# Performance work log

Measured on AMD Instinct MI355X. Metric: run time of the kernel, lower is better.

Reference implementation:

```python
import jax, jax.numpy as jnp
import numpy as np

NUM_EXPERTS = 64
TOP_K = 8
HIDDEN = 2048
MLP = 768
TOKENS = 1024


def setup_inputs() -> dict:
    key = jax.random.key(0)
    ks = jax.random.split(key, 5)
    hidden_states = jax.random.normal(ks[0], (TOKENS, HIDDEN), dtype=jnp.float32)
    # lecun-normal-ish scaling (std = 1/sqrt(fan_in))
    router_w = jax.random.normal(ks[1], (HIDDEN, NUM_EXPERTS), dtype=jnp.float32) / np.sqrt(HIDDEN)
    gate_proj = jax.random.normal(ks[2], (NUM_EXPERTS, HIDDEN, MLP), dtype=jnp.float32) / np.sqrt(HIDDEN)
    up_proj = jax.random.normal(ks[3], (NUM_EXPERTS, HIDDEN, MLP), dtype=jnp.float32) / np.sqrt(HIDDEN)
    down_proj = jax.random.normal(ks[4], (NUM_EXPERTS, MLP, HIDDEN), dtype=jnp.float32) / np.sqrt(MLP)
    return {
        "hidden_states": hidden_states,
        "router_w": router_w,
        "gate_proj": gate_proj,
        "up_proj": up_proj,
        "down_proj": down_proj,
    }


def reference(hidden_states, router_w, gate_proj, up_proj, down_proj):
    # Router: [T, E]
    router_logits = hidden_states @ router_w
    # Top-k routing, softmax renormalized over the selected k (norm_topk_prob=True)
    routing_weights, selected_experts = jax.lax.top_k(router_logits, k=TOP_K)
    routing_weights = jax.nn.softmax(routing_weights, axis=-1)  # [T, k]

    sel_flat = selected_experts.ravel()  # [T*k] int32
    # Duplicate each token for each of its k experts: [T*k, H]
    x_exp = jnp.repeat(hidden_states, TOP_K, axis=0)

    # prepare_routing: sort token copies by expert id, count per-expert group sizes
    sort_idx = jnp.argsort(sel_flat)          # stable sort of expert ids
    x_sorted = x_exp[sort_idx]                # [T*k, H] grouped by expert
    group_sizes = jnp.zeros((NUM_EXPERTS,), dtype=jnp.int32).at[sel_flat].add(1)
    unsort_idx = jnp.argsort(sort_idx)

    # Grouped GEMMs (megablox-style) via ragged_dot
    gate_out = jax.lax.ragged_dot(x_sorted, gate_proj, group_sizes)   # [T*k, M]
    up_out = jax.lax.ragged_dot(x_sorted, up_proj, group_sizes)       # [T*k, M]
    down_out = jax.lax.ragged_dot(jax.nn.silu(gate_out) * up_out, down_proj, group_sizes)  # [T*k, H]

    # Unsort back to (token, k) order and combine with routing weights
    unsorted = down_out[unsort_idx].reshape(-1, TOP_K, HIDDEN)
    return jnp.sum(unsorted * routing_weights[..., None], axis=1)  # [T, H]
```

## Files before the change

kernel.cpp:

```cpp
#include <hip/hip_runtime.h>
#include <hip/hip_bf16.h>

#define T_TOKENS 1024
#define HID      2048
#define NEXP     64
#define TOPK     8
#define MLP      768
#define NPAIR    (T_TOKENS * TOPK)

typedef __bf16 bf16x8 __attribute__((ext_vector_type(8)));
typedef float  f32x4  __attribute__((ext_vector_type(4)));
typedef unsigned int u32x2 __attribute__((ext_vector_type(2)));
typedef unsigned int u32x4 __attribute__((ext_vector_type(4)));

#define LDK 40

static __device__ __forceinline__ unsigned short f2bf(float f) {
    __hip_bfloat16 h = __float2bfloat16(f);
    unsigned short u;
    __builtin_memcpy(&u, &h, sizeof(u));
    return u;
}
static __device__ __forceinline__ unsigned int pk2bf(float a, float b) {
    return (unsigned int)f2bf(a) | ((unsigned int)f2bf(b) << 16);
}

__global__ __launch_bounds__(256) void router_topk_kernel(
    const float* __restrict__ hs, const float* __restrict__ rw,
    int* __restrict__ sel, float* __restrict__ wts, unsigned short* __restrict__ xb)
{
    const int lane = threadIdx.x & 63;
    const int tg   = threadIdx.x >> 6;
    const int t    = blockIdx.x * 4 + tg;

    {
        const float* xr = hs + (size_t)t * HID;
        unsigned short* xw = xb + (size_t)t * HID;
        #pragma unroll
        for (int c = 0; c < 4; ++c) {
            int i = (lane + c * 64) * 8;
            f32x4 a = *(const f32x4*)(xr + i);
            f32x4 b = *(const f32x4*)(xr + i + 4);
            u32x4 v;
            v[0] = pk2bf(a[0], a[1]); v[1] = pk2bf(a[2], a[3]);
            v[2] = pk2bf(b[0], b[1]); v[3] = pk2bf(b[2], b[3]);
            *(u32x4*)(xw + i) = v;
        }
    }

    const float4* x4 = (const float4*)(hs + (size_t)t * HID);
    float acc = 0.f;
    for (int h4 = 0; h4 < HID / 4; ++h4) {
        float4 xv = x4[h4];
        int hb = h4 * 4 * NEXP + lane;
        acc += xv.x * rw[hb] + xv.y * rw[hb + NEXP]
             + xv.z * rw[hb + 2 * NEXP] + xv.w * rw[hb + 3 * NEXP];
    }

    float v = acc;
    float tv[TOPK]; int ti[TOPK];
    for (int i = 0; i < TOPK; ++i) {
        float m = v; int mi = lane;
        for (int off = 32; off > 0; off >>= 1) {
            float om  = __shfl_xor(m, off, 64);
            int   omi = __shfl_xor(mi, off, 64);
            if (om > m || (om == m && omi < mi)) { m = om; mi = omi; }
        }
        tv[i] = m; ti[i] = mi;
        if (lane == mi) v = -__builtin_inff();
    }
    if (lane == 0) {
        float mx = tv[0], s = 0.f, e[TOPK];
        for (int i = 0; i < TOPK; ++i) { e[i] = __expf(tv[i] - mx); s += e[i]; }
        float inv = 1.f / s;
        for (int i = 0; i < TOPK; ++i) {
            wts[t * TOPK + i] = e[i] * inv;
            sel[t * TOPK + i] = ti[i];
        }
    }
}

__global__ __launch_bounds__(1024) void route_kernel(
    const int* __restrict__ sel, int* __restrict__ offsets, int* __restrict__ rows)
{
    __shared__ int cnt[NEXP];
    __shared__ int cur[NEXP];
    const int t = threadIdx.x;
    if (t < NEXP) cnt[t] = 0;
    __syncthreads();
    int e[8];
    const int p0 = t * 8;
    #pragma unroll
    for (int j = 0; j < 8; ++j) {
        e[j] = sel[p0 + j];
        atomicAdd(&cnt[e[j]], 1);
    }
    __syncthreads();
    if (t == 0) {
        int s = 0;
        for (int i = 0; i < NEXP; ++i) { cur[i] = s; offsets[i] = s; s += cnt[i]; }
        offsets[NEXP] = s;
    }
    __syncthreads();
    #pragma unroll
    for (int j = 0; j < 8; ++j) {
        int pos = atomicAdd(&cur[e[j]], 1);
        rows[pos] = p0 + j;
    }
}

__global__ __launch_bounds__(256, 2) void gateup_kernel(
    const unsigned short* __restrict__ xb, const float* __restrict__ gw,
    const float* __restrict__ uw, const int* __restrict__ offsets,
    const int* __restrict__ rows, unsigned short* __restrict__ hb)
{
    const int bid = blockIdx.x;
    const int sw  = (bid & 7) * 96 + (bid >> 3);
    const int e   = sw / 12;
    const int n0  = (sw % 12) * 64;

    const int r0 = offsets[e];
    const int nrows = offsets[e + 1] - r0;
    if (nrows <= 0) return;

    __shared__ __align__(16) float smemf[12800];
    unsigned short* smem = (unsigned short*)smemf;

    const int thr  = threadIdx.x;
    const int wave = thr >> 6;
    const int lane = thr & 63;
    const int wg   = wave & 1;
    const int isUp = wave >> 1;
    const int fr   = lane & 15;
    const int fq   = lane >> 4;
    const int mofs_c = isUp ? 10240 : 7680;

    const int ar = thr >> 2;
    const int ac = (thr & 3) * 8;

    const int tt   = thr & 127;
    const int wk2  = tt & 15;
    const int nst  = (tt >> 4) * 8;
    const float* wsrc = (thr >= 128 ? uw : gw)
        + (size_t)e * HID * MLP + (size_t)(2 * wk2) * MLP + n0 + nst;
    const int mofs_s = (thr >= 128) ? 10240 : 7680;

    const int NS = HID / 32;

    for (int m0 = 0; m0 < nrows; m0 += 192) {
        const unsigned short *ap0, *ap1, *ap2;
        bool av0, av1, av2;
        {
            int gr0 = m0 + ar, gr1 = m0 + ar + 64, gr2 = m0 + ar + 128;
            av0 = gr0 < nrows; av1 = gr1 < nrows; av2 = gr2 < nrows;
            int p0 = av0 ? rows[r0 + gr0] : 0;
            int p1 = av1 ? rows[r0 + gr1] : 0;
            int p2 = av2 ? rows[r0 + gr2] : 0;
            ap0 = xb + (size_t)(p0 >> 3) * HID + ac;
            ap1 = xb + (size_t)(p1 >> 3) * HID + ac;
            ap2 = xb + (size_t)(p2 >> 3) * HID + ac;
        }

        u32x4 va0, va1, va2;
        f32x4 wAe, wBe, wCe, wDe, wAo, wBo, wCo, wDo;
        const u32x4 uz = (u32x4){0u, 0u, 0u, 0u};
        const f32x4 fz = (f32x4){0.f, 0.f, 0.f, 0.f};

        auto LOAD_A = [&](int s) {
            va0 = av0 ? *(const u32x4*)(ap0 + s * 32) : uz;
            va1 = av1 ? *(const u32x4*)(ap1 + s * 32) : uz;
            va2 = av2 ? *(const u32x4*)(ap2 + s * 32) : uz;
        };
        auto WRITE_A = [&](int s) {
            unsigned short* b = smem + (s & 1) * 12800;
            *(u32x4*)(b + ar * LDK + ac) = va0;
            *(u32x4*)(b + (ar + 64) * LDK + ac) = va1;
            *(u32x4*)(b + (ar + 128) * LDK + ac) = va2;
        };
        auto LOAD_WE = [&](int s) {
            const float* wp = wsrc + (size_t)s * 32 * MLP;
            wAe = *(const f32x4*)wp;        wBe = *(const f32x4*)(wp + 4);
            wCe = *(const f32x4*)(wp + MLP); wDe = *(const f32x4*)(wp + MLP + 4);
        };
        auto LOAD_WO = [&](int s) {
            const float* wp = wsrc + (size_t)s * 32 * MLP;
            wAo = *(const f32x4*)wp;        wBo = *(const f32x4*)(wp + 4);
            wCo = *(const f32x4*)(wp + MLP); wDo = *(const f32x4*)(wp + MLP + 4);
        };
        auto WRITE_WE = [&](int s) {
            unsigned short* wb = smem + (s & 1) * 12800 + mofs_s;
            #pragma unroll
            for (int j = 0; j < 4; ++j) {
                *(unsigned int*)(wb + (nst + j) * LDK + 2 * wk2)     = pk2bf(wAe[j], wCe[j]);
                *(unsigned int*)(wb + (nst + 4 + j) * LDK + 2 * wk2) = pk2bf(wBe[j], wDe[j]);
            }
        };
        auto WRITE_WO = [&](int s) {
            unsigned short* wb = smem + (s & 1) * 12800 + mofs_s;
            #pragma unroll
            for (int j = 0; j < 4; ++j) {
                *(unsigned int*)(wb + (nst + j) * LDK + 2 * wk2)     = pk2bf(wAo[j], wCo[j]);
                *(unsigned int*)(wb + (nst + 4 + j) * LDK + 2 * wk2) = pk2bf(wBo[j], wDo[j]);
            }
        };

        f32x4 acc[6][4];
        #pragma unroll
        for (int ms = 0; ms < 6; ++ms)
            #pragma unroll
            for (int ns = 0; ns < 4; ++ns) acc[ms][ns] = fz;

        const int rem = nrows - m0 - wg * 96;

        auto STEP = [&](const unsigned short* bb) {
            const unsigned short* wbb = bb + mofs_c;
            bf16x8 wF0 = *(const bf16x8*)(wbb + (0 * 16 + fr) * LDK + fq * 8);
            bf16x8 wF1 = *(const bf16x8*)(wbb + (1 * 16 + fr) * LDK + fq * 8);
            bf16x8 wF2 = *(const bf16x8*)(wbb + (2 * 16 + fr) * LDK + fq * 8);
            bf16x8 wF3 = *(const bf16x8*)(wbb + (3 * 16 + fr) * LDK + fq * 8);
            bf16x8 aF[6];
            #pragma unroll
            for (int ms = 0; ms < 6; ++ms)
                aF[ms] = *(const bf16x8*)(bb + (wg * 96 + ms * 16 + fr) * LDK + fq * 8);
            #pragma unroll
            for (int ms = 0; ms < 6; ++ms) {
                if (rem > ms * 16) {
                    acc[ms][0] = __builtin_amdgcn_mfma_f32_16x16x32_bf16(aF[ms], wF0, acc[ms][0], 0, 0, 0);
                    acc[ms][1] = __builtin_amdgcn_mfma_f32_16x16x32_bf16(aF[ms], wF1, acc[ms][1], 0, 0, 0);
                    acc[ms][2] = __builtin_amdgcn_mfma_f32_16x16x32_bf16(aF[ms], wF2, acc[ms][2], 0, 0, 0);
                    acc[ms][3] = __builtin_amdgcn_mfma_f32_16x16x32_bf16(aF[ms], wF3, acc[ms][3], 0, 0, 0);
                }
            }
        };

        LOAD_WE(0);
        LOAD_WO(1);
        LOAD_A(0);
        WRITE_WE(0);
        WRITE_A(0);
        LOAD_A(1);
        asm volatile("s_waitcnt lgkmcnt(0)" ::: "memory");
        __builtin_amdgcn_s_barrier();

        for (int s = 0; s < NS; s += 2) {
            if (s + 2 < NS) LOAD_WE(s + 2);
            STEP(smem);
            WRITE_WO(s + 1);
            WRITE_A(s + 1);
            if (s + 2 < NS) LOAD_A(s + 2);
            asm volatile("s_waitcnt lgkmcnt(0)" ::: "memory");
            __builtin_amdgcn_s_barrier();
            if (s + 3 < NS) LOAD_WO(s + 3);
            STEP(smem + 12800);
            if (s + 2 < NS) { WRITE_WE(s + 2); WRITE_A(s + 2); }
            if (s + 3 < NS) LOAD_A(s + 3);
            asm volatile("s_waitcnt lgkmcnt(0)" ::: "memory");
            __builtin_amdgcn_s_barrier();
        }

        float* xbf = smemf;
        if (isUp) {
            #pragma unroll
            for (int ms = 0; ms < 6; ++ms)
                #pragma unroll
                for (int i = 0; i < 4; ++i) {
                    int lrow = wg * 96 + ms * 16 + fq * 4 + i;
                    #pragma unroll
                    for (int ns = 0; ns < 4; ++ns)
                        xbf[lrow * 65 + ns * 16 + fr] = acc[ms][ns][i];
                }
        }
        __syncthreads();
        if (!isUp) {
            #pragma unroll
            for (int ms = 0; ms < 6; ++ms)
                #pragma unroll
                for (int i = 0; i < 4; ++i) {
                    int lrow = wg * 96 + ms * 16 + fq * 4 + i;
                    int grow = m0 + lrow;
                    if (grow < nrows) {
                        unsigned short* drow = hb + (size_t)(r0 + grow) * MLP + n0;
                        #pragma unroll
                        for (int ns = 0; ns < 4; ++ns) {
                            float g = acc[ms][ns][i];
                            float u = xbf[lrow * 65 + ns * 16 + fr];
                            float h = g * u / (1.f + __expf(-g));
                            drow[ns * 16 + fr] = f2bf(h);
                        }
                    }
                }
        }
        __syncthreads();
    }
}

__global__ __launch_bounds__(256, 2) void down_kernel(
    const unsigned short* __restrict__ hb, const float* __restrict__ dw,
    const int* __restrict__ offsets, const int* __restrict__ rows,
    const float* __restrict__ wts, float* __restrict__ out)
{
    const int bid = blockIdx.x;
    const int sw  = (bid & 7) * 128 + (bid >> 3);
    const int e   = sw >> 4;
    const int n0  = (sw & 15) * 128;

    const int r0 = offsets[e];
    const int nrows = offsets[e + 1] - r0;
    if (nrows <= 0) return;

    __shared__ __align__(16) float smemf[12800];
    unsigned short* smem = (unsigned short*)smemf;

    const int thr  = threadIdx.x;
    const int wave = thr >> 6;
    const int lane = thr & 63;
    const int wg   = wave & 1;
    const int wn   = wave >> 1;
    const int fr   = lane & 15;
    const int fq   = lane >> 4;

    const int ar = thr >> 2;
    const int ac = (thr & 3) * 8;

    const int wk2 = thr & 15;
    const int nst = (thr >> 4) * 8;
    const float* wsrc = dw + (size_t)e * MLP * HID + (size_t)(2 * wk2) * HID + n0 + nst;

    const int NS = MLP / 32;

    for (int m0 = 0; m0 < nrows; m0 += 192) {
        const bool av0 = (m0 + ar)       < nrows;
        const bool av1 = (m0 + ar + 64)  < nrows;
        const bool av2 = (m0 + ar + 128) < nrows;
        const unsigned short* hp0 = hb + (size_t)(r0 + m0 + ar) * MLP + ac;
        const unsigned short* hp1 = hp0 + (size_t)64  * MLP;
        const unsigned short* hp2 = hp0 + (size_t)128 * MLP;

        u32x4 ua0, ua1, ua2;
        f32x4 wAe, wBe, wCe, wDe, wAo, wBo, wCo, wDo;
        const u32x4 uz = (u32x4){0u, 0u, 0u, 0u};
        const f32x4 fz = (f32x4){0.f, 0.f, 0.f, 0.f};

        auto LOAD_A = [&](int s) {
            ua0 = av0 ? *(const u32x4*)(hp0 + s * 32) : uz;
            ua1 = av1 ? *(const u32x4*)(hp1 + s * 32) : uz;
            ua2 = av2 ? *(const u32x4*)(hp2 + s * 32) : uz;
        };
        auto WRITE_A = [&](int s) {
            unsigned short* b = smem + (s & 1) * 12800;
            *(u32x4*)(b + ar * LDK + ac) = ua0;
            *(u32x4*)(b + (ar + 64) * LDK + ac) = ua1;
            *(u32x4*)(b + (ar + 128) * LDK + ac) = ua2;
        };
        auto LOAD_WE = [&](int s) {
            const float* wp = wsrc + (size_t)s * 32 * HID;
            wAe = *(const f32x4*)wp;        wBe = *(const f32x4*)(wp + 4);
            wCe = *(const f32x4*)(wp + HID); wDe = *(const f32x4*)(wp + HID + 4);
        };
        auto LOAD_WO = [&](int s) {
            const float* wp = wsrc + (size_t)s * 32 * HID;
            wAo = *(const f32x4*)wp;        wBo = *(const f32x4*)(wp + 4);
            wCo = *(const f32x4*)(wp + HID); wDo = *(const f32x4*)(wp + HID + 4);
        };
        auto WRITE_WE = [&](int s) {
            unsigned short* wb = smem + (s & 1) * 12800 + 7680;
            #pragma unroll
            for (int j = 0; j < 4; ++j) {
                *(unsigned int*)(wb + (nst + j) * LDK + 2 * wk2)     = pk2bf(wAe[j], wCe[j]);
                *(unsigned int*)(wb + (nst + 4 + j) * LDK + 2 * wk2) = pk2bf(wBe[j], wDe[j]);
            }
        };
        auto WRITE_WO = [&](int s) {
            unsigned short* wb = smem + (s & 1) * 12800 + 7680;
            #pragma unroll
            for (int j = 0; j < 4; ++j) {
                *(unsigned int*)(wb + (nst + j) * LDK + 2 * wk2)     = pk2bf(wAo[j], wCo[j]);
                *(unsigned int*)(wb + (nst + 4 + j) * LDK + 2 * wk2) = pk2bf(wBo[j], wDo[j]);
            }
        };

        f32x4 acc[6][4];
        #pragma unroll
        for (int ms = 0; ms < 6; ++ms)
            #pragma unroll
            for (int ns = 0; ns < 4; ++ns) acc[ms][ns] = fz;

        const int rem = nrows - m0 - wg * 96;

        auto STEP = [&](const unsigned short* bb) {
            const unsigned short* wbb = bb + 7680;
            bf16x8 wF0 = *(const bf16x8*)(wbb + (wn * 64 + 0 * 16 + fr) * LDK + fq * 8);
            bf16x8 wF1 = *(const bf16x8*)(wbb + (wn * 64 + 1 * 16 + fr) * LDK + fq * 8);
            bf16x8 wF2 = *(const bf16x8*)(wbb + (wn * 64 + 2 * 16 + fr) * LDK + fq * 8);
            bf16x8 wF3 = *(const bf16x8*)(wbb + (wn * 64 + 3 * 16 + fr) * LDK + fq * 8);
            bf16x8 aF[6];
            #pragma unroll
            for (int ms = 0; ms < 6; ++ms)
                aF[ms] = *(const bf16x8*)(bb + (wg * 96 + ms * 16 + fr) * LDK + fq * 8);
            #pragma unroll
            for (int ms = 0; ms < 6; ++ms) {
                if (rem > ms * 16) {
                    acc[ms][0] = __builtin_amdgcn_mfma_f32_16x16x32_bf16(aF[ms], wF0, acc[ms][0], 0, 0, 0);
                    acc[ms][1] = __builtin_amdgcn_mfma_f32_16x16x32_bf16(aF[ms], wF1, acc[ms][1], 0, 0, 0);
                    acc[ms][2] = __builtin_amdgcn_mfma_f32_16x16x32_bf16(aF[ms], wF2, acc[ms][2], 0, 0, 0);
                    acc[ms][3] = __builtin_amdgcn_mfma_f32_16x16x32_bf16(aF[ms], wF3, acc[ms][3], 0, 0, 0);
                }
            }
        };

        LOAD_WE(0);
        LOAD_WO(1);
        LOAD_A(0);
        WRITE_WE(0);
        WRITE_A(0);
        LOAD_A(1);
        asm volatile("s_waitcnt lgkmcnt(0)" ::: "memory");
        __builtin_amdgcn_s_barrier();

        for (int s = 0; s < NS; s += 2) {
            if (s + 2 < NS) LOAD_WE(s + 2);
            STEP(smem);
            WRITE_WO(s + 1);
            WRITE_A(s + 1);
            if (s + 2 < NS) LOAD_A(s + 2);
            asm volatile("s_waitcnt lgkmcnt(0)" ::: "memory");
            __builtin_amdgcn_s_barrier();
            if (s + 3 < NS) LOAD_WO(s + 3);
            STEP(smem + 12800);
            if (s + 2 < NS) { WRITE_WE(s + 2); WRITE_A(s + 2); }
            if (s + 3 < NS) LOAD_A(s + 3);
            asm volatile("s_waitcnt lgkmcnt(0)" ::: "memory");
            __builtin_amdgcn_s_barrier();
        }

        #pragma unroll
        for (int ms = 0; ms < 6; ++ms) {
            #pragma unroll
            for (int i = 0; i < 4; ++i) {
                int lrow = wg * 96 + ms * 16 + fq * 4 + i;
                int grow = m0 + lrow;
                if (grow < nrows) {
                    int p  = rows[r0 + grow];
                    float w = wts[p];
                    float* orow = out + (size_t)(p >> 3) * HID + n0 + wn * 64;
                    #pragma unroll
                    for (int ns = 0; ns < 4; ++ns)
                        atomicAdd(orow + ns * 16 + fr, acc[ms][ns][i] * w);
                }
            }
        }
        __syncthreads();
    }
}

extern "C" void kernel_launch(void* const* d_in, const int* in_sizes, int n_in,
                              void* d_out, int out_size, void* d_ws, size_t ws_size,
                              hipStream_t stream)
{
    const float* hs = (const float*)d_in[0];
    const float* rw = (const float*)d_in[1];
    const float* gw = (const float*)d_in[2];
    const float* uw = (const float*)d_in[3];
    const float* dw = (const float*)d_in[4];
    float* out = (float*)d_out;

    char* ws = (char*)d_ws;
    int*   sel     = (int*)(ws);
    float* wts     = (float*)(ws + 32768);
    int*   offsets = (int*)(ws + 65792);
    int*   rows    = (int*)(ws + 66560);
    unsigned short* xb = (unsigned short*)(ws + 99328);
    unsigned short* hb = (unsigned short*)(ws + 99328 + 4194304);

    hipMemsetAsync(out, 0, (size_t)T_TOKENS * HID * sizeof(float), stream);

    router_topk_kernel<<<T_TOKENS / 4, 256, 0, stream>>>(hs, rw, sel, wts, xb);
    route_kernel<<<1, 1024, 0, stream>>>(sel, offsets, rows);
    gateup_kernel<<<768, 256, 0, stream>>>(xb, gw, uw, offsets, rows, hb);
    down_kernel<<<1024, 256, 0, stream>>>(hb, dw, offsets, rows, wts, out);
}
```

Measured before the change: 1.198 ms.

## Load activation fragments straight from global memory into registers, shrink LDS tiles

Both grouped GEMM kernels stop staging the activation rows in LDS. Each wave now loads its bf16 A fragments directly from global memory into registers, double-buffered even/odd, and only the fp32→bf16 converted weight tile goes through LDS. Gate/up blocks grow to 512 threads with 48 rows per wave, and the down kernel is split into 64-wide N tiles across twice as many blocks. The intent is to cut LDS traffic and footprint to raise occupancy. In exchange, the A rows are re-read from global or L2 by every wave that needs them, and more blocks issue atomic adds to the output.

```diff
diff --git a/kernel.cpp b/kernel.cpp
--- a/kernel.cpp
+++ b/kernel.cpp
@@ -10,7 +10,6 @@
 
 typedef __bf16 bf16x8 __attribute__((ext_vector_type(8)));
 typedef float  f32x4  __attribute__((ext_vector_type(4)));
-typedef unsigned int u32x2 __attribute__((ext_vector_type(2)));
 typedef unsigned int u32x4 __attribute__((ext_vector_type(4)));
 
 #define LDK 40
@@ -109,7 +108,7 @@
     }
 }
 
-__global__ __launch_bounds__(256, 2) void gateup_kernel(
+__global__ __launch_bounds__(512, 4) void gateup_kernel(
     const unsigned short* __restrict__ xb, const float* __restrict__ gw,
     const float* __restrict__ uw, const int* __restrict__ offsets,
     const int* __restrict__ rows, unsigned short* __restrict__ hb)
@@ -123,107 +122,84 @@
     const int nrows = offsets[e + 1] - r0;
     if (nrows <= 0) return;
 
-    __shared__ __align__(16) float smemf[12800];
-    unsigned short* smem = (unsigned short*)smemf;
+    __shared__ __align__(16) unsigned short smem[2 * 5120];
 
     const int thr  = threadIdx.x;
     const int wave = thr >> 6;
     const int lane = thr & 63;
-    const int wg   = wave & 1;
-    const int isUp = wave >> 1;
+    const int wg   = wave & 3;
+    const int isUp = wave >> 2;
     const int fr   = lane & 15;
     const int fq   = lane >> 4;
-    const int mofs_c = isUp ? 10240 : 7680;
-
-    const int ar = thr >> 2;
-    const int ac = (thr & 3) * 8;
-
-    const int tt   = thr & 127;
+    const int mofs_c = isUp ? 2560 : 0;
+
+    const int tt   = thr & 255;
     const int wk2  = tt & 15;
-    const int nst  = (tt >> 4) * 8;
-    const float* wsrc = (thr >= 128 ? uw : gw)
-        + (size_t)e * HID * MLP + (size_t)(2 * wk2) * MLP + n0 + nst;
-    const int mofs_s = (thr >= 128) ? 10240 : 7680;
+    const int wnq  = tt >> 4;
+    const float* wsrc = (thr >= 256 ? uw : gw)
+        + (size_t)e * HID * MLP + (size_t)(2 * wk2) * MLP + n0 + wnq * 4;
+    const int mofs_s = (thr >= 256) ? 2560 : 0;
 
     const int NS = HID / 32;
 
     for (int m0 = 0; m0 < nrows; m0 += 192) {
-        const unsigned short *ap0, *ap1, *ap2;
-        bool av0, av1, av2;
-        {
-            int gr0 = m0 + ar, gr1 = m0 + ar + 64, gr2 = m0 + ar + 128;
-            av0 = gr0 < nrows; av1 = gr1 < nrows; av2 = gr2 < nrows;
-            int p0 = av0 ? rows[r0 + gr0] : 0;
-            int p1 = av1 ? rows[r0 + gr1] : 0;
-            int p2 = av2 ? rows[r0 + gr2] : 0;
-            ap0 = xb + (size_t)(p0 >> 3) * HID + ac;
-            ap1 = xb + (size_t)(p1 >> 3) * HID + ac;
-            ap2 = xb + (size_t)(p2 >> 3) * HID + ac;
-        }
-
-        u32x4 va0, va1, va2;
-        f32x4 wAe, wBe, wCe, wDe, wAo, wBo, wCo, wDo;
-        const u32x4 uz = (u32x4){0u, 0u, 0u, 0u};
-        const f32x4 fz = (f32x4){0.f, 0.f, 0.f, 0.f};
-
-        auto LOAD_A = [&](int s) {
-            va0 = av0 ? *(const u32x4*)(ap0 + s * 32) : uz;
-            va1 = av1 ? *(const u32x4*)(ap1 + s * 32) : uz;
-            va2 = av2 ? *(const u32x4*)(ap2 + s * 32) : uz;
-        };
-        auto WRITE_A = [&](int s) {
-            unsigned short* b = smem + (s & 1) * 12800;
-            *(u32x4*)(b + ar * LDK + ac) = va0;
-            *(u32x4*)(b + (ar + 64) * LDK + ac) = va1;
-            *(u32x4*)(b + (ar + 128) * LDK + ac) = va2;
+        const unsigned short* apf[3];
+        #pragma unroll
+        for (int ms = 0; ms < 3; ++ms) {
+            int r = m0 + wg * 48 + ms * 16 + fr;
+            if (r > nrows - 1) r = nrows - 1;
+            int p = rows[r0 + r];
+            apf[ms] = xb + (size_t)(p >> 3) * HID + fq * 8;
+        }
+
+        bf16x8 aE[3], aO[3];
+        f32x4 w0e, w1e, w0o, w1o;
+
+        auto LOAD_AE = [&](int s) {
+            #pragma unroll
+            for (int ms = 0; ms < 3; ++ms) aE[ms] = *(const bf16x8*)(apf[ms] + s * 32);
+        };
+        auto LOAD_AO = [&](int s) {
+            #pragma unroll
+            for (int ms = 0; ms < 3; ++ms) aO[ms] = *(const bf16x8*)(apf[ms] + s * 32);
         };
         auto LOAD_WE = [&](int s) {
             const float* wp = wsrc + (size_t)s * 32 * MLP;
-            wAe = *(const f32x4*)wp;        wBe = *(const f32x4*)(wp + 4);
-            wCe = *(const f32x4*)(wp + MLP); wDe = *(const f32x4*)(wp + MLP + 4);
+            w0e = *(const f32x4*)wp;  w1e = *(const f32x4*)(wp + MLP);
         };
         auto LOAD_WO = [&](int s) {
             const float* wp = wsrc + (size_t)s * 32 * MLP;
-            wAo = *(const f32x4*)wp;        wBo = *(const f32x4*)(wp + 4);
-            wCo = *(const f32x4*)(wp + MLP); wDo = *(const f32x4*)(wp + MLP + 4);
+            w0o = *(const f32x4*)wp;  w1o = *(const f32x4*)(wp + MLP);
         };
         auto WRITE_WE = [&](int s) {
-            unsigned short* wb = smem + (s & 1) * 12800 + mofs_s;
-            #pragma unroll
-            for (int j = 0; j < 4; ++j) {
-                *(unsigned int*)(wb + (nst + j) * LDK + 2 * wk2)     = pk2bf(wAe[j], wCe[j]);
-                *(unsigned int*)(wb + (nst + 4 + j) * LDK + 2 * wk2) = pk2bf(wBe[j], wDe[j]);
-            }
+            unsigned short* wb = smem + (s & 1) * 5120 + mofs_s;
+            #pragma unroll
+            for (int i = 0; i < 4; ++i)
+                *(unsigned int*)(wb + (wnq * 4 + i) * LDK + 2 * wk2) = pk2bf(w0e[i], w1e[i]);
         };
         auto WRITE_WO = [&](int s) {
-            unsigned short* wb = smem + (s & 1) * 12800 + mofs_s;
-            #pragma unroll
-            for (int j = 0; j < 4; ++j) {
-                *(unsigned int*)(wb + (nst + j) * LDK + 2 * wk2)     = pk2bf(wAo[j], wCo[j]);
-                *(unsigned int*)(wb + (nst + 4 + j) * LDK + 2 * wk2) = pk2bf(wBo[j], wDo[j]);
-            }
-        };
-
-        f32x4 acc[6][4];
-        #pragma unroll
-        for (int ms = 0; ms < 6; ++ms)
-            #pragma unroll
-            for (int ns = 0; ns < 4; ++ns) acc[ms][ns] = fz;
-
-        const int rem = nrows - m0 - wg * 96;
-
-        auto STEP = [&](const unsigned short* bb) {
-            const unsigned short* wbb = bb + mofs_c;
+            unsigned short* wb = smem + (s & 1) * 5120 + mofs_s;
+            #pragma unroll
+            for (int i = 0; i < 4; ++i)
+                *(unsigned int*)(wb + (wnq * 4 + i) * LDK + 2 * wk2) = pk2bf(w0o[i], w1o[i]);
+        };
+
+        f32x4 acc[3][4];
+        #pragma unroll
+        for (int ms = 0; ms < 3; ++ms)
+            #pragma unroll
+            for (int ns = 0; ns < 4; ++ns) acc[ms][ns] = (f32x4){0.f, 0.f, 0.f, 0.f};
+
+        const int rem = nrows - m0 - wg * 48;
+
+        auto STEP = [&](const unsigned short* buf, bf16x8* aF) {
+            const unsigned short* wbb = buf + mofs_c;
             bf16x8 wF0 = *(const bf16x8*)(wbb + (0 * 16 + fr) * LDK + fq * 8);
             bf16x8 wF1 = *(const bf16x8*)(wbb + (1 * 16 + fr) * LDK + fq * 8);
             bf16x8 wF2 = *(const bf16x8*)(wbb + (2 * 16 + fr) * LDK + fq * 8);
             bf16x8 wF3 = *(const bf16x8*)(wbb + (3 * 16 + fr) * LDK + fq * 8);
-            bf16x8 aF[6];
-            #pragma unroll
-            for (int ms = 0; ms < 6; ++ms)
-                aF[ms] = *(const bf16x8*)(bb + (wg * 96 + ms * 16 + fr) * LDK + fq * 8);
-            #pragma unroll
-            for (int ms = 0; ms < 6; ++ms) {
+            #pragma unroll
+            for (int ms = 0; ms < 3; ++ms) {
                 if (rem > ms * 16) {
                     acc[ms][0] = __builtin_amdgcn_mfma_f32_16x16x32_bf16(aF[ms], wF0, acc[ms][0], 0, 0, 0);
                     acc[ms][1] = __builtin_amdgcn_mfma_f32_16x16x32_bf16(aF[ms], wF1, acc[ms][1], 0, 0, 0);
@@ -235,170 +211,146 @@
 
         LOAD_WE(0);
         LOAD_WO(1);
-        LOAD_A(0);
+        LOAD_AE(0);
         WRITE_WE(0);
-        WRITE_A(0);
-        LOAD_A(1);
+        LOAD_AO(1);
         asm volatile("s_waitcnt lgkmcnt(0)" ::: "memory");
         __builtin_amdgcn_s_barrier();
 
         for (int s = 0; s < NS; s += 2) {
             if (s + 2 < NS) LOAD_WE(s + 2);
-            STEP(smem);
+            STEP(smem, aE);
+            if (s + 2 < NS) LOAD_AE(s + 2);
             WRITE_WO(s + 1);
-            WRITE_A(s + 1);
-            if (s + 2 < NS) LOAD_A(s + 2);
             asm volatile("s_waitcnt lgkmcnt(0)" ::: "memory");
             __builtin_amdgcn_s_barrier();
             if (s + 3 < NS) LOAD_WO(s + 3);
-            STEP(smem + 12800);
-            if (s + 2 < NS) { WRITE_WE(s + 2); WRITE_A(s + 2); }
-            if (s + 3 < NS) LOAD_A(s + 3);
+            STEP(smem + 5120, aO);
+            if (s + 3 < NS) LOAD_AO(s + 3);
+            if (s + 2 < NS) WRITE_WE(s + 2);
             asm volatile("s_waitcnt lgkmcnt(0)" ::: "memory");
             __builtin_amdgcn_s_barrier();
         }
 
-        float* xbf = smemf;
-        if (isUp) {
-            #pragma unroll
-            for (int ms = 0; ms < 6; ++ms)
+        float* xbf = (float*)smem;
+        #pragma unroll
+        for (int ms = 0; ms < 3; ++ms) {
+            if (isUp) {
                 #pragma unroll
                 for (int i = 0; i < 4; ++i) {
-                    int lrow = wg * 96 + ms * 16 + fq * 4 + i;
+                    int xrow = wg * 16 + fq * 4 + i;
                     #pragma unroll
                     for (int ns = 0; ns < 4; ++ns)
-                        xbf[lrow * 65 + ns * 16 + fr] = acc[ms][ns][i];
+                        xbf[xrow * 65 + ns * 16 + fr] = acc[ms][ns][i];
                 }
-        }
-        __syncthreads();
-        if (!isUp) {
-            #pragma unroll
-            for (int ms = 0; ms < 6; ++ms)
+            }
+            __syncthreads();
+            if (!isUp) {
                 #pragma unroll
                 for (int i = 0; i < 4; ++i) {
-                    int lrow = wg * 96 + ms * 16 + fq * 4 + i;
-                    int grow = m0 + lrow;
+                    int xrow = wg * 16 + fq * 4 + i;
+                    int grow = m0 + wg * 48 + ms * 16 + fq * 4 + i;
                     if (grow < nrows) {
                         unsigned short* drow = hb + (size_t)(r0 + grow) * MLP + n0;
                         #pragma unroll
                         for (int ns = 0; ns < 4; ++ns) {
                             float g = acc[ms][ns][i];
-                            float u = xbf[lrow * 65 + ns * 16 + fr];
+                            float u = xbf[xrow * 65 + ns * 16 + fr];
                             float h = g * u / (1.f + __expf(-g));
                             drow[ns * 16 + fr] = f2bf(h);
                         }
                     }
                 }
-        }
-        __syncthreads();
-    }
-}
-
-__global__ __launch_bounds__(256, 2) void down_kernel(
+            }
+            __syncthreads();
+        }
+    }
+}
+
+__global__ __launch_bounds__(256, 4) void down_kernel(
     const unsigned short* __restrict__ hb, const float* __restrict__ dw,
     const int* __restrict__ offsets, const int* __restrict__ rows,
     const float* __restrict__ wts, float* __restrict__ out)
 {
     const int bid = blockIdx.x;
-    const int sw  = (bid & 7) * 128 + (bid >> 3);
-    const int e   = sw >> 4;
-    const int n0  = (sw & 15) * 128;
+    const int sw  = (bid & 7) * 256 + (bid >> 3);
+    const int e   = sw >> 5;
+    const int n0  = (sw & 31) * 64;
 
     const int r0 = offsets[e];
     const int nrows = offsets[e + 1] - r0;
     if (nrows <= 0) return;
 
-    __shared__ __align__(16) float smemf[12800];
-    unsigned short* smem = (unsigned short*)smemf;
+    __shared__ __align__(16) unsigned short smem[2 * 2560];
 
     const int thr  = threadIdx.x;
     const int wave = thr >> 6;
     const int lane = thr & 63;
-    const int wg   = wave & 1;
-    const int wn   = wave >> 1;
     const int fr   = lane & 15;
     const int fq   = lane >> 4;
 
-    const int ar = thr >> 2;
-    const int ac = (thr & 3) * 8;
-
     const int wk2 = thr & 15;
-    const int nst = (thr >> 4) * 8;
-    const float* wsrc = dw + (size_t)e * MLP * HID + (size_t)(2 * wk2) * HID + n0 + nst;
+    const int wnq = thr >> 4;
+    const float* wsrc = dw + (size_t)e * MLP * HID + (size_t)(2 * wk2) * HID + n0 + wnq * 4;
 
     const int NS = MLP / 32;
 
     for (int m0 = 0; m0 < nrows; m0 += 192) {
-        const bool av0 = (m0 + ar)       < nrows;
-        const bool av1 = (m0 + ar + 64)  < nrows;
-        const bool av2 = (m0 + ar + 128) < nrows;
-        const unsigned short* hp0 = hb + (size_t)(r0 + m0 + ar) * MLP + ac;
-        const unsigned short* hp1 = hp0 + (size_t)64  * MLP;
-        const unsigned short* hp2 = hp0 + (size_t)128 * MLP;
-
-        u32x4 ua0, ua1, ua2;
-        f32x4 wAe, wBe, wCe, wDe, wAo, wBo, wCo, wDo;
-        const u32x4 uz = (u32x4){0u, 0u, 0u, 0u};
-        const f32x4 fz = (f32x4){0.f, 0.f, 0.f, 0.f};
-
-        auto LOAD_A = [&](int s) {
-            ua0 = av0 ? *(const u32x4*)(hp0 + s * 32) : uz;
-            ua1 = av1 ? *(const u32x4*)(hp1 + s * 32) : uz;
-            ua2 = av2 ? *(const u32x4*)(hp2 + s * 32) : uz;
-        };
-        auto WRITE_A = [&](int s) {
-            unsigned short* b = smem + (s & 1) * 12800;
-            *(u32x4*)(b + ar * LDK + ac) = ua0;
-            *(u32x4*)(b + (ar + 64) * LDK + ac) = ua1;
-            *(u32x4*)(b + (ar + 128) * LDK + ac) = ua2;
+        const unsigned short* apf[3];
+        #pragma unroll
+        for (int ms = 0; ms < 3; ++ms) {
+            int r = m0 + wave * 48 + ms * 16 + fr;
+            if (r > nrows - 1) r = nrows - 1;
+            apf[ms] = hb + (size_t)(r0 + r) * MLP + fq * 8;
+        }
+
+        bf16x8 aE[3], aO[3];
+        f32x4 w0e, w1e, w0o, w1o;
+
+        auto LOAD_AE = [&](int s) {
+            #pragma unroll
+            for (int ms = 0; ms < 3; ++ms) aE[ms] = *(const bf16x8*)(apf[ms] + s * 32);
+        };
+        auto LOAD_AO = [&](int s) {
+            #pragma unroll
+            for (int ms = 0; ms < 3; ++ms) aO[ms] = *(const bf16x8*)(apf[ms] + s * 32);
         };
         auto LOAD_WE = [&](int s) {
             const float* wp = wsrc + (size_t)s * 32 * HID;
-            wAe = *(const f32x4*)wp;        wBe = *(const f32x4*)(wp + 4);
-            wCe = *(const f32x4*)(wp + HID); wDe = *(const f32x4*)(wp + HID + 4);
+            w0e = *(const f32x4*)wp;  w1e = *(const f32x4*)(wp + HID);
         };
         auto LOAD_WO = [&](int s) {
             const float* wp = wsrc + (size_t)s * 32 * HID;
-            wAo = *(const f32x4*)wp;        wBo = *(const f32x4*)(wp + 4);
-            wCo = *(const f32x4*)(wp + HID); wDo = *(const f32x4*)(wp + HID + 4);
+            w0o = *(const f32x4*)wp;  w1o = *(const f32x4*)(wp + HID);
         };
         auto WRITE_WE = [&](int s) {
-            unsigned short* wb = smem + (s & 1) * 12800 + 7680;
-            #pragma unroll
-            for (int j = 0; j < 4; ++j) {
-                *(unsigned int*)(wb + (nst + j) * LDK + 2 * wk2)     = pk2bf(wAe[j], wCe[j]);
-                *(unsigned int*)(wb + (nst + 4 + j) * LDK + 2 * wk2) = pk2bf(wBe[j], wDe[j]);
-            }
+            unsigned short* wb = smem + (s & 1) * 2560;
+            #pragma unroll
+            for (int i = 0; i < 4; ++i)
+                *(unsigned int*)(wb + (wnq * 4 + i) * LDK + 2 * wk2) = pk2bf(w0e[i], w1e[i]);
         };
         auto WRITE_WO = [&](int s) {
-            unsigned short* wb = smem + (s & 1) * 12800 + 7680;
-            #pragma unroll
-            for (int j = 0; j < 4; ++j) {
-                *(unsigned int*)(wb + (nst + j) * LDK + 2 * wk2)     = pk2bf(wAo[j], wCo[j]);
-                *(unsigned int*)(wb + (nst + 4 + j) * LDK + 2 * wk2) = pk2bf(wBo[j], wDo[j]);
-            }
-        };
-
-        f32x4 acc[6][4];
-        #pragma unroll
-        for (int ms = 0; ms < 6; ++ms)
-            #pragma unroll
-            for (int ns = 0; ns < 4; ++ns) acc[ms][ns] = fz;
-
-        const int rem = nrows - m0 - wg * 96;
-
-        auto STEP = [&](const unsigned short* bb) {
-            const unsigned short* wbb = bb + 7680;
-            bf16x8 wF0 = *(const bf16x8*)(wbb + (wn * 64 + 0 * 16 + fr) * LDK + fq * 8);
-            bf16x8 wF1 = *(const bf16x8*)(wbb + (wn * 64 + 1 * 16 + fr) * LDK + fq * 8);
-            bf16x8 wF2 = *(const bf16x8*)(wbb + (wn * 64 + 2 * 16 + fr) * LDK + fq * 8);
-            bf16x8 wF3 = *(const bf16x8*)(wbb + (wn * 64 + 3 * 16 + fr) * LDK + fq * 8);
-            bf16x8 aF[6];
-            #pragma unroll
-            for (int ms = 0; ms < 6; ++ms)
-                aF[ms] = *(const bf16x8*)(bb + (wg * 96 + ms * 16 + fr) * LDK + fq * 8);
-            #pragma unroll
-            for (int ms = 0; ms < 6; ++ms) {
+            unsigned short* wb = smem + (s & 1) * 2560;
+            #pragma unroll
+            for (int i = 0; i < 4; ++i)
+                *(unsigned int*)(wb + (wnq * 4 + i) * LDK + 2 * wk2) = pk2bf(w0o[i], w1o[i]);
+        };
+
+        f32x4 acc[3][4];
+        #pragma unroll
+        for (int ms = 0; ms < 3; ++ms)
+            #pragma unroll
+            for (int ns = 0; ns < 4; ++ns) acc[ms][ns] = (f32x4){0.f, 0.f, 0.f, 0.f};
+
+        const int rem = nrows - m0 - wave * 48;
+
+        auto STEP = [&](const unsigned short* buf, bf16x8* aF) {
+            bf16x8 wF0 = *(const bf16x8*)(buf + (0 * 16 + fr) * LDK + fq * 8);
+            bf16x8 wF1 = *(const bf16x8*)(buf + (1 * 16 + fr) * LDK + fq * 8);
+            bf16x8 wF2 = *(const bf16x8*)(buf + (2 * 16 + fr) * LDK + fq * 8);
+            bf16x8 wF3 = *(const bf16x8*)(buf + (3 * 16 + fr) * LDK + fq * 8);
+            #pragma unroll
+            for (int ms = 0; ms < 3; ++ms) {
                 if (rem > ms * 16) {
                     acc[ms][0] = __builtin_amdgcn_mfma_f32_16x16x32_bf16(aF[ms], wF0, acc[ms][0], 0, 0, 0);
                     acc[ms][1] = __builtin_amdgcn_mfma_f32_16x16x32_bf16(aF[ms], wF1, acc[ms][1], 0, 0, 0);
@@ -410,39 +362,36 @@
 
         LOAD_WE(0);
         LOAD_WO(1);
-        LOAD_A(0);
+        LOAD_AE(0);
         WRITE_WE(0);
-        WRITE_A(0);
-        LOAD_A(1);
+        LOAD_AO(1);
         asm volatile("s_waitcnt lgkmcnt(0)" ::: "memory");
         __builtin_amdgcn_s_barrier();
 
         for (int s = 0; s < NS; s += 2) {
             if (s + 2 < NS) LOAD_WE(s + 2);
-            STEP(smem);
+            STEP(smem, aE);
+            if (s + 2 < NS) LOAD_AE(s + 2);
             WRITE_WO(s + 1);
-            WRITE_A(s + 1);
-            if (s + 2 < NS) LOAD_A(s + 2);
             asm volatile("s_waitcnt lgkmcnt(0)" ::: "memory");
             __builtin_amdgcn_s_barrier();
             if (s + 3 < NS) LOAD_WO(s + 3);
-            STEP(smem + 12800);
-            if (s + 2 < NS) { WRITE_WE(s + 2); WRITE_A(s + 2); }
-            if (s + 3 < NS) LOAD_A(s + 3);
+            STEP(smem + 2560, aO);
+            if (s + 3 < NS) LOAD_AO(s + 3);
+            if (s + 2 < NS) WRITE_WE(s + 2);
             asm volatile("s_waitcnt lgkmcnt(0)" ::: "memory");
             __builtin_amdgcn_s_barrier();
         }
 
         #pragma unroll
-        for (int ms = 0; ms < 6; ++ms) {
+        for (int ms = 0; ms < 3; ++ms) {
             #pragma unroll
             for (int i = 0; i < 4; ++i) {
-                int lrow = wg * 96 + ms * 16 + fq * 4 + i;
-                int grow = m0 + lrow;
+                int grow = m0 + wave * 48 + ms * 16 + fq * 4 + i;
                 if (grow < nrows) {
                     int p  = rows[r0 + grow];
                     float w = wts[p];
-                    float* orow = out + (size_t)(p >> 3) * HID + n0 + wn * 64;
+                    float* orow = out + (size_t)(p >> 3) * HID + n0;
                     #pragma unroll
                     for (int ns = 0; ns < 4; ++ns)
                         atomicAdd(orow + ns * 16 + fr, acc[ms][ns][i] * w);
@@ -476,6 +425,6 @@
 
     router_topk_kernel<<<T_TOKENS / 4, 256, 0, stream>>>(hs, rw, sel, wts, xb);
     route_kernel<<<1, 1024, 0, stream>>>(sel, offsets, rows);
-    gateup_kernel<<<768, 256, 0, stream>>>(xb, gw, uw, offsets, rows, hb);
-    down_kernel<<<1024, 256, 0, stream>>>(hb, dw, offsets, rows, wts, out);
-}
+    gateup_kernel<<<768, 512, 0, stream>>>(xb, gw, uw, offsets, rows, hb);
+    down_kernel<<<2048, 256, 0, stream>>>(hb, dw, offsets, rows, wts, out);
+}
```

Result: slower. 1.260 ms (+5.2%).
